# Optimization experiments

Measured on AMD Instinct MI355X. Metric: run time of the kernel, lower is better.

The kernel has to match this reference:

```python
import jax, jax.numpy as jnp
import numpy as np

HEADS = 4
DIM_HEAD = 32
DIM = 128
HIDDEN = HEADS * DIM_HEAD  # 128


def setup_inputs() -> dict:
    key = jax.random.key(0)
    k1, k2, k3, k4 = jax.random.split(key, 4)
    B, C, H, W = 8, DIM, 128, 128
    x = jax.random.normal(k1, (B, C, H, W), dtype=jnp.float32)
    # 1x1 conv weights stored as [out_ch, in_ch] (kernel dims squeezed)
    w_qkv = jax.random.normal(k2, (3 * HIDDEN, DIM), dtype=jnp.float32) * (1.0 / np.sqrt(DIM))
    w_out = jax.random.normal(k3, (DIM, HIDDEN), dtype=jnp.float32) * (1.0 / np.sqrt(HIDDEN))
    b_out = jax.random.normal(k4, (DIM,), dtype=jnp.float32) * 0.01
    return {"x": x, "w_qkv": w_qkv, "w_out": w_out, "b_out": b_out}


def reference(x, w_qkv, w_out, b_out):
    b, c, h, w = x.shape
    n = h * w
    # 1x1 conv == per-pixel matmul over channels
    qkv = jnp.einsum('bchw,oc->bohw', x, w_qkv)            # [b, 3*HIDDEN, h, w]
    # channel layout: (qkv, heads, dim_head)
    qkv = qkv.reshape(b, 3, HEADS, DIM_HEAD, n)            # [b, 3, H, d, n]
    q, k, v = qkv[:, 0], qkv[:, 1], qkv[:, 2]
    k = jax.nn.softmax(k, axis=-1)                         # softmax over spatial n
    context = jnp.einsum('bhdn,bhen->bhde', k, v)          # [b, H, d, d] (tiny)
    out = jnp.einsum('bhde,bhdn->bhen', context, q)        # [b, H, d, n]
    out = out.reshape(b, HIDDEN, h, w)
    y = jnp.einsum('bchw,oc->bohw', out, w_out) + b_out[None, :, None, None]
    return y
```

## Files before the change

kernel.cpp:

```cpp
#include <hip/hip_runtime.h>
#include <math.h>

#define C_ 128
#define N_ 16384

#define WS_Z    0
#define WS_CTX  1024
#define WS_BMAT 33792
#define WS_A    164864
#define WS_PCTX 295936
#define WS_PZ   (WS_PCTX + 1024*4096)
#define WS_END  (WS_PZ + 512*128)

typedef __attribute__((ext_vector_type(8))) short bf16x8;
typedef __attribute__((ext_vector_type(4))) float f32x4;
typedef __attribute__((ext_vector_type(4))) unsigned int u32x4;

__device__ __forceinline__ unsigned int pkbf(float a, float b) {
  unsigned int r;
  asm("v_cvt_pk_bf16_f32 %0, %1, %2" : "=v"(r) : "v"(a), "v"(b));
  return r;
}

__device__ __forceinline__ bf16x8 make_frag(float4 u, float4 v) {
  u32x4 q = {pkbf(u.x, u.y), pkbf(u.z, u.w), pkbf(v.x, v.y), pkbf(v.z, v.w)};
  return *(bf16x8*)&q;
}

__device__ __forceinline__ bf16x8 lds_frag(const unsigned short* p) {
  bf16x8 f;
  ((unsigned long long*)&f)[0] = ((const unsigned long long*)p)[0];
  ((unsigned long long*)&f)[1] = ((const unsigned long long*)p)[1];
  return f;
}

template<bool ATOMIC>
__global__ __launch_bounds__(512, 4) void k1_kv_ctx(const float* __restrict__ x,
                                                    const float* __restrict__ wqkv,
                                                    float* __restrict__ ws) {
  __shared__ __attribute__((aligned(16))) unsigned short smem[2 * 128 * 68];
#define XS(n, c)    smem[(n) * 132 + (c)]
#define EKV(t, r, c) smem[((t) * 128 + (r)) * 68 + (c)]
  const int tid  = threadIdx.x;
  const int wave = tid >> 6;
  const int l15  = tid & 15;
  const int l4   = (tid >> 4) & 3;
  const int b    = blockIdx.y;
  const int j    = blockIdx.x;
  const int h    = wave & 3;
  const int t    = wave >> 2;
  const int kvrow0 = h * 32 + t * 128;
  const float* xb = x + (size_t)b * ((size_t)C_ * N_);

  bf16x8 wf[2][4];
  #pragma unroll
  for (int mi = 0; mi < 2; ++mi)
    #pragma unroll
    for (int ki = 0; ki < 4; ++ki) {
      const float* p = wqkv + (size_t)(128 + kvrow0 + mi * 16 + l15) * C_ + ki * 32 + l4 * 8;
      wf[mi][ki] = make_frag(*(const float4*)p, *(const float4*)(p + 4));
    }

  const f32x4 z4 = {0.f, 0.f, 0.f, 0.f};
  f32x4 ctxacc[2][2];
  #pragma unroll
  for (int i = 0; i < 2; ++i)
    #pragma unroll
    for (int jj = 0; jj < 2; ++jj) ctxacc[i][jj] = z4;
  float zacc[2][4];
  #pragma unroll
  for (int i = 0; i < 2; ++i)
    #pragma unroll
    for (int r = 0; r < 4; ++r) zacc[i][r] = 0.f;

  for (int st = 0; st < 4; ++st) {
    const int nb = j * 256 + st * 64;
    __syncthreads();
    #pragma unroll
    for (int i = 0; i < 4; ++i) {
      int idx = tid + i * 512;
      int k = idx >> 4, n4 = idx & 15;
      float4 v = *(const float4*)(xb + (size_t)k * N_ + nb + n4 * 4);
      unsigned int p01 = pkbf(v.x, v.y), p23 = pkbf(v.z, v.w);
      XS(n4 * 4 + 0, k) = (unsigned short)p01;
      XS(n4 * 4 + 1, k) = (unsigned short)(p01 >> 16);
      XS(n4 * 4 + 2, k) = (unsigned short)p23;
      XS(n4 * 4 + 3, k) = (unsigned short)(p23 >> 16);
    }
    __syncthreads();

    f32x4 acc[2][4];
    #pragma unroll
    for (int mi = 0; mi < 2; ++mi)
      #pragma unroll
      for (int ni = 0; ni < 4; ++ni) acc[mi][ni] = z4;
    #pragma unroll
    for (int ki = 0; ki < 4; ++ki) {
      bf16x8 bfr[4];
      #pragma unroll
      for (int ni = 0; ni < 4; ++ni)
        bfr[ni] = lds_frag(&XS(ni * 16 + l15, ki * 32 + l4 * 8));
      #pragma unroll
      for (int mi = 0; mi < 2; ++mi)
        #pragma unroll
        for (int ni = 0; ni < 4; ++ni)
          acc[mi][ni] = __builtin_amdgcn_mfma_f32_16x16x32_bf16(
              wf[mi][ki], bfr[ni], acc[mi][ni], 0, 0, 0);
    }
    __syncthreads();

    #pragma unroll
    for (int mi = 0; mi < 2; ++mi) {
      int rb = h * 32 + mi * 16 + l4 * 4;
      #pragma unroll
      for (int ni = 0; ni < 4; ++ni) {
        int col = ni * 16 + l15;
        float e0, e1, e2, e3;
        if (t == 0) {
          e0 = __expf(acc[mi][ni][0]); e1 = __expf(acc[mi][ni][1]);
          e2 = __expf(acc[mi][ni][2]); e3 = __expf(acc[mi][ni][3]);
          zacc[mi][0] += e0; zacc[mi][1] += e1;
          zacc[mi][2] += e2; zacc[mi][3] += e3;
        } else {
          e0 = acc[mi][ni][0]; e1 = acc[mi][ni][1];
          e2 = acc[mi][ni][2]; e3 = acc[mi][ni][3];
        }
        unsigned int p01 = pkbf(e0, e1), p23 = pkbf(e2, e3);
        EKV(t, rb + 0, col) = (unsigned short)p01;
        EKV(t, rb + 1, col) = (unsigned short)(p01 >> 16);
        EKV(t, rb + 2, col) = (unsigned short)p23;
        EKV(t, rb + 3, col) = (unsigned short)(p23 >> 16);
      }
    }
    __syncthreads();

    {
      bf16x8 af[2], bfv[2];
      #pragma unroll
      for (int m2 = 0; m2 < 2; ++m2)
        af[m2] = lds_frag(&EKV(0, h * 32 + m2 * 16 + l15, t * 32 + l4 * 8));
      #pragma unroll
      for (int n2 = 0; n2 < 2; ++n2)
        bfv[n2] = lds_frag(&EKV(1, h * 32 + n2 * 16 + l15, t * 32 + l4 * 8));
      #pragma unroll
      for (int m2 = 0; m2 < 2; ++m2)
        #pragma unroll
        for (int n2 = 0; n2 < 2; ++n2)
          ctxacc[m2][n2] = __builtin_amdgcn_mfma_f32_16x16x32_bf16(
              af[m2], bfv[n2], ctxacc[m2][n2], 0, 0, 0);
    }
  }

  if (!ATOMIC) {
    float* ps = ws + WS_PCTX + (size_t)((b * 64 + j) * 2 + t) * 4096 + h * 1024;
    #pragma unroll
    for (int m2 = 0; m2 < 2; ++m2)
      #pragma unroll
      for (int n2 = 0; n2 < 2; ++n2)
        #pragma unroll
        for (int r = 0; r < 4; ++r)
          ps[(m2 * 16 + l4 * 4 + r) * 32 + n2 * 16 + l15] = ctxacc[m2][n2][r];
  } else {
    float* ctx = ws + WS_CTX + (size_t)(b * 4 + h) * 1024;
    #pragma unroll
    for (int m2 = 0; m2 < 2; ++m2)
      #pragma unroll
      for (int n2 = 0; n2 < 2; ++n2)
        #pragma unroll
        for (int r = 0; r < 4; ++r)
          atomicAdd(&ctx[(m2 * 16 + l4 * 4 + r) * 32 + n2 * 16 + l15],
                    ctxacc[m2][n2][r]);
  }
  if (t == 0) {
    #pragma unroll
    for (int mi = 0; mi < 2; ++mi)
      #pragma unroll
      for (int r = 0; r < 4; ++r) {
        float z = zacc[mi][r];
        z += __shfl_xor(z, 1);
        z += __shfl_xor(z, 2);
        z += __shfl_xor(z, 4);
        z += __shfl_xor(z, 8);
        if (l15 == 0) {
          int row = h * 32 + mi * 16 + l4 * 4 + r;
          if (!ATOMIC)
            ws[WS_PZ + (size_t)(b * 64 + j) * 128 + row] = z;
          else
            atomicAdd(&ws[WS_Z + b * 128 + row], z);
        }
      }
  }
#undef XS
#undef EKV
}

__global__ __launch_bounds__(256) void k1b(float* __restrict__ ws) {
  const int tid = threadIdx.x;
  const int eq = blockIdx.x;
  const int h  = blockIdx.y;
  const int b  = blockIdx.z;
  const int el = eq * 256 + tid;
  const float* p = ws + WS_PCTX + (size_t)(b * 128) * 4096 + h * 1024 + el;
  float s = 0.f;
  #pragma unroll 8
  for (int jj = 0; jj < 128; ++jj) s += p[(size_t)jj * 4096];
  ws[WS_CTX + (size_t)(b * 4 + h) * 1024 + el] = s;
  if (eq == 0 && tid < 32) {
    const float* pz = ws + WS_PZ + (size_t)(b * 64) * 128 + h * 32 + tid;
    float z = 0.f;
    #pragma unroll 8
    for (int jj = 0; jj < 64; ++jj) z += pz[(size_t)jj * 128];
    ws[WS_Z + b * 128 + h * 32 + tid] = z;
  }
}

__global__ __launch_bounds__(256) void k2a(const float* __restrict__ w_qkv,
                                           float* __restrict__ ws) {
  __shared__ float cn[32][33];
  __shared__ float wqs[32][128];
  const int tid = threadIdx.x;
  const int h = blockIdx.x, b = blockIdx.y;
  const float* Z   = ws + WS_Z + b * 128 + h * 32;
  const float* ctx = ws + WS_CTX + ((b * 4 + h) * 32) * 32;

  for (int k = 0; k < 4; ++k) {
    int idx = tid + k * 256;
    int d = idx >> 5, e = idx & 31;
    cn[d][e] = ctx[d * 32 + e] / Z[d];
  }
  for (int k = 0; k < 4; ++k) {
    int idx = tid + k * 256;
    int d = idx >> 5, f4 = idx & 31;
    *(float4*)&wqs[d][f4 * 4] = *(const float4*)(w_qkv + (h * 32 + d) * 128 + f4 * 4);
  }
  __syncthreads();

  const int e = tid >> 3, cs = (tid & 7) * 16;
  float s[16];
  #pragma unroll
  for (int jj = 0; jj < 16; ++jj) s[jj] = 0.f;
  for (int d = 0; d < 32; ++d) {
    float v = cn[d][e];
    #pragma unroll
    for (int jj = 0; jj < 16; ++jj) s[jj] = fmaf(v, wqs[d][cs + jj], s[jj]);
  }
  float* Bm = ws + WS_BMAT + ((size_t)b * 128 + h * 32 + e) * 128;
  #pragma unroll
  for (int jj = 0; jj < 16; ++jj) Bm[cs + jj] = s[jj];
}

__global__ __launch_bounds__(256) void k2b(const float* __restrict__ w_out,
                                           float* __restrict__ ws) {
  __shared__ float bs[128][128];
  __shared__ float wos[32][128];
  const int tid = threadIdx.x;
  const int oq = blockIdx.x, b = blockIdx.y;
  const float* Bm = ws + WS_BMAT + (size_t)b * 128 * 128;

  for (int k = 0; k < 16; ++k) {
    int idx = tid + k * 256;
    int r = idx >> 5, f4 = idx & 31;
    *(float4*)&bs[r][f4 * 4] = *(const float4*)(Bm + r * 128 + f4 * 4);
  }
  for (int k = 0; k < 4; ++k) {
    int idx = tid + k * 256;
    int r = idx >> 5, f4 = idx & 31;
    *(float4*)&wos[r][f4 * 4] = *(const float4*)(w_out + (oq * 32 + r) * 128 + f4 * 4);
  }
  __syncthreads();

  const int ol = tid >> 3, cq = (tid & 7) * 16;
  float s[16];
  #pragma unroll
  for (int jj = 0; jj < 16; ++jj) s[jj] = 0.f;
  for (int eg = 0; eg < 128; ++eg) {
    float w = wos[ol][eg];
    #pragma unroll
    for (int jj = 0; jj < 16; ++jj) s[jj] = fmaf(w, bs[eg][cq + jj], s[jj]);
  }
  float* A = ws + WS_A + ((size_t)b * 128 + oq * 32 + ol) * 128;
  #pragma unroll
  for (int jj = 0; jj < 16; ++jj) A[cq + jj] = s[jj];
}

__global__ __launch_bounds__(256, 4) void k3(const float* __restrict__ x,
                                             const float* __restrict__ bout,
                                             const float* __restrict__ ws,
                                             float* __restrict__ y) {
  __shared__ __attribute__((aligned(16))) unsigned short xs2[2][64][132];
  const int tid  = threadIdx.x;
  const int wave = tid >> 6;
  const int l15  = tid & 15;
  const int l4   = (tid >> 4) & 3;
  const int b    = blockIdx.y;
  const int n0   = blockIdx.x * 128;
  const float* xb = x + (size_t)b * ((size_t)C_ * N_);
  const float* A  = ws + WS_A + (size_t)b * 128 * 128;

  bf16x8 af[2][4];
  #pragma unroll
  for (int mi = 0; mi < 2; ++mi)
    #pragma unroll
    for (int ki = 0; ki < 4; ++ki) {
      const float* p = A + (size_t)(wave * 32 + mi * 16 + l15) * 128 + ki * 32 + l4 * 8;
      af[mi][ki] = make_frag(*(const float4*)p, *(const float4*)(p + 4));
    }
  float bias[2][4];
  #pragma unroll
  for (int mi = 0; mi < 2; ++mi)
    #pragma unroll
    for (int r = 0; r < 4; ++r)
      bias[mi][r] = bout[wave * 32 + mi * 16 + l4 * 4 + r];

  #pragma unroll
  for (int i = 0; i < 8; ++i) {
    int idx = tid + i * 256;
    int k = idx >> 4, n4 = idx & 15;
    float4 v = *(const float4*)(xb + (size_t)k * N_ + n0 + n4 * 4);
    unsigned int p01 = pkbf(v.x, v.y), p23 = pkbf(v.z, v.w);
    xs2[0][n4 * 4 + 0][k] = (unsigned short)p01;
    xs2[0][n4 * 4 + 1][k] = (unsigned short)(p01 >> 16);
    xs2[0][n4 * 4 + 2][k] = (unsigned short)p23;
    xs2[0][n4 * 4 + 3][k] = (unsigned short)(p23 >> 16);
  }
  __syncthreads();

  const f32x4 z4 = {0.f, 0.f, 0.f, 0.f};
  float* yb = y + (size_t)b * ((size_t)128 * N_);

  #pragma unroll
  for (int st = 0; st < 2; ++st) {
    const int nb = n0 + st * 64;
    f32x4 acc[2][4];
    #pragma unroll
    for (int mi = 0; mi < 2; ++mi)
      #pragma unroll
      for (int ni = 0; ni < 4; ++ni) acc[mi][ni] = z4;
    #pragma unroll
    for (int ki = 0; ki < 4; ++ki) {
      bf16x8 bfr[4];
      #pragma unroll
      for (int ni = 0; ni < 4; ++ni)
        bfr[ni] = lds_frag(&xs2[st][ni * 16 + l15][ki * 32 + l4 * 8]);
      #pragma unroll
      for (int mi = 0; mi < 2; ++mi)
        #pragma unroll
        for (int ni = 0; ni < 4; ++ni)
          acc[mi][ni] = __builtin_amdgcn_mfma_f32_16x16x32_bf16(
              af[mi][ki], bfr[ni], acc[mi][ni], 0, 0, 0);
    }

    if (st == 0) {
      #pragma unroll
      for (int i = 0; i < 8; ++i) {
        int idx = tid + i * 256;
        int k = idx >> 4, n4 = idx & 15;
        float4 v = *(const float4*)(xb + (size_t)k * N_ + n0 + 64 + n4 * 4);
        unsigned int p01 = pkbf(v.x, v.y), p23 = pkbf(v.z, v.w);
        xs2[1][n4 * 4 + 0][k] = (unsigned short)p01;
        xs2[1][n4 * 4 + 1][k] = (unsigned short)(p01 >> 16);
        xs2[1][n4 * 4 + 2][k] = (unsigned short)p23;
        xs2[1][n4 * 4 + 3][k] = (unsigned short)(p23 >> 16);
      }
    }

    #pragma unroll
    for (int mi = 0; mi < 2; ++mi)
      #pragma unroll
      for (int ni = 0; ni < 4; ++ni)
        #pragma unroll
        for (int r = 0; r < 4; ++r)
          yb[(size_t)(wave * 32 + mi * 16 + l4 * 4 + r) * N_ + nb + ni * 16 + l15] =
              acc[mi][ni][r] + bias[mi][r];

    if (st == 0) __syncthreads();
  }
}

extern "C" void kernel_launch(void* const* d_in, const int* in_sizes, int n_in,
                              void* d_out, int out_size, void* d_ws, size_t ws_size,
                              hipStream_t stream) {
  const float* x     = (const float*)d_in[0];
  const float* w_qkv = (const float*)d_in[1];
  const float* w_out = (const float*)d_in[2];
  const float* b_out = (const float*)d_in[3];
  float* y  = (float*)d_out;
  float* ws = (float*)d_ws;

  const bool partial = ws_size >= (size_t)WS_END * sizeof(float);
  if (partial) {
    k1_kv_ctx<false><<<dim3(64, 8), 512, 0, stream>>>(x, w_qkv, ws);
    k1b<<<dim3(4, 4, 8), 256, 0, stream>>>(ws);
  } else {
    hipMemsetAsync(ws, 0, (1024 + 32768) * sizeof(float), stream);
    k1_kv_ctx<true><<<dim3(64, 8), 512, 0, stream>>>(x, w_qkv, ws);
  }
  k2a<<<dim3(4, 8), 256, 0, stream>>>(w_qkv, ws);
  k2b<<<dim3(4, 8), 256, 0, stream>>>(w_out, ws);
  k3<<<dim3(128, 8), 256, 0, stream>>>(x, b_out, ws, y);
}
```

Measured before the change: 89.29 us.

## Swap MFMA operand order, vectorize LDS/global stores, prefetch x tiles in KV kernel

The MFMA operands are swapped so each lane holds four consecutive spatial outputs. This lets the exp(k)/v tile be written to LDS as 8-byte vectors and the final y output be written as float4 rows instead of scalar strided stores. The x tile transpose into LDS now packs four channels per 8-byte store, and LDS row padding changes to 136/72. The KV kernel register-prefetches the next x tile during compute, removes one barrier per step, and lowers its occupancy hint from 4 to 2 blocks per CU, which adds register pressure.

```diff
diff --git a/kernel.cpp b/kernel.cpp
--- a/kernel.cpp
+++ b/kernel.cpp
@@ -15,6 +15,7 @@
 typedef __attribute__((ext_vector_type(8))) short bf16x8;
 typedef __attribute__((ext_vector_type(4))) float f32x4;
 typedef __attribute__((ext_vector_type(4))) unsigned int u32x4;
+typedef __attribute__((ext_vector_type(2))) unsigned int u32x2;
 
 __device__ __forceinline__ unsigned int pkbf(float a, float b) {
   unsigned int r;
@@ -27,20 +28,22 @@
   return *(bf16x8*)&q;
 }
 
-__device__ __forceinline__ bf16x8 lds_frag(const unsigned short* p) {
-  bf16x8 f;
-  ((unsigned long long*)&f)[0] = ((const unsigned long long*)p)[0];
-  ((unsigned long long*)&f)[1] = ((const unsigned long long*)p)[1];
-  return f;
+__device__ __forceinline__ bf16x8 lds_frag16(const unsigned short* p) {
+  u32x4 q = *(const u32x4*)p;
+  return *(bf16x8*)&q;
+}
+
+__device__ __forceinline__ void load4(const float* p, float* o) {
+  float4 v = *(const float4*)p;
+  o[0] = v.x; o[1] = v.y; o[2] = v.z; o[3] = v.w;
 }
 
 template<bool ATOMIC>
-__global__ __launch_bounds__(512, 4) void k1_kv_ctx(const float* __restrict__ x,
+__global__ __launch_bounds__(512, 2) void k1_kv_ctx(const float* __restrict__ x,
                                                     const float* __restrict__ wqkv,
                                                     float* __restrict__ ws) {
-  __shared__ __attribute__((aligned(16))) unsigned short smem[2 * 128 * 68];
-#define XS(n, c)    smem[(n) * 132 + (c)]
-#define EKV(t, r, c) smem[((t) * 128 + (r)) * 68 + (c)]
+  __shared__ __attribute__((aligned(16))) unsigned short xs[64][136];
+  __shared__ __attribute__((aligned(16))) unsigned short ekv[2][128][72];
   const int tid  = threadIdx.x;
   const int wave = tid >> 6;
   const int l15  = tid & 15;
@@ -52,6 +55,9 @@
   const int kvrow0 = h * 32 + t * 128;
   const float* xb = x + (size_t)b * ((size_t)C_ * N_);
 
+  const int sn4 = tid & 15;
+  const int scq = tid >> 4;
+
   bf16x8 wf[2][4];
   #pragma unroll
   for (int mi = 0; mi < 2; ++mi)
@@ -61,94 +67,99 @@
       wf[mi][ki] = make_frag(*(const float4*)p, *(const float4*)(p + 4));
     }
 
+  {
+    float va[4][4];
+    #pragma unroll
+    for (int r = 0; r < 4; ++r)
+      load4(xb + (size_t)(scq * 4 + r) * N_ + j * 256 + sn4 * 4, va[r]);
+    #pragma unroll
+    for (int i = 0; i < 4; ++i) {
+      u32x2 w = {pkbf(va[0][i], va[1][i]), pkbf(va[2][i], va[3][i])};
+      *(u32x2*)&xs[sn4 * 4 + i][scq * 4] = w;
+    }
+  }
+  __syncthreads();
+
   const f32x4 z4 = {0.f, 0.f, 0.f, 0.f};
   f32x4 ctxacc[2][2];
   #pragma unroll
   for (int i = 0; i < 2; ++i)
     #pragma unroll
     for (int jj = 0; jj < 2; ++jj) ctxacc[i][jj] = z4;
-  float zacc[2][4];
-  #pragma unroll
-  for (int i = 0; i < 2; ++i)
-    #pragma unroll
-    for (int r = 0; r < 4; ++r) zacc[i][r] = 0.f;
+  float zacc[2] = {0.f, 0.f};
 
   for (int st = 0; st < 4; ++st) {
-    const int nb = j * 256 + st * 64;
+    float pf[4][4];
+    if (st < 3) {
+      const int nbn = j * 256 + (st + 1) * 64;
+      #pragma unroll
+      for (int r = 0; r < 4; ++r)
+        load4(xb + (size_t)(scq * 4 + r) * N_ + nbn + sn4 * 4, pf[r]);
+    }
+
+    #pragma unroll
+    for (int half = 0; half < 2; ++half) {
+      f32x4 acc[2][2];
+      #pragma unroll
+      for (int a = 0; a < 2; ++a)
+        #pragma unroll
+        for (int m = 0; m < 2; ++m) acc[a][m] = z4;
+      #pragma unroll
+      for (int ki = 0; ki < 4; ++ki) {
+        bf16x8 bfr[2];
+        #pragma unroll
+        for (int ni2 = 0; ni2 < 2; ++ni2)
+          bfr[ni2] = lds_frag16(&xs[half * 32 + ni2 * 16 + l15][ki * 32 + l4 * 8]);
+        #pragma unroll
+        for (int ni2 = 0; ni2 < 2; ++ni2)
+          #pragma unroll
+          for (int mi = 0; mi < 2; ++mi)
+            acc[ni2][mi] = __builtin_amdgcn_mfma_f32_16x16x32_bf16(
+                bfr[ni2], wf[mi][ki], acc[ni2][mi], 0, 0, 0);
+      }
+      #pragma unroll
+      for (int ni2 = 0; ni2 < 2; ++ni2)
+        #pragma unroll
+        for (int mi = 0; mi < 2; ++mi) {
+          float e0, e1, e2, e3;
+          if (t == 0) {
+            e0 = __expf(acc[ni2][mi][0]); e1 = __expf(acc[ni2][mi][1]);
+            e2 = __expf(acc[ni2][mi][2]); e3 = __expf(acc[ni2][mi][3]);
+            zacc[mi] += (e0 + e1) + (e2 + e3);
+          } else {
+            e0 = acc[ni2][mi][0]; e1 = acc[ni2][mi][1];
+            e2 = acc[ni2][mi][2]; e3 = acc[ni2][mi][3];
+          }
+          u32x2 w = {pkbf(e0, e1), pkbf(e2, e3)};
+          *(u32x2*)&ekv[t][h * 32 + mi * 16 + l15][(half * 2 + ni2) * 16 + l4 * 4] = w;
+        }
+    }
     __syncthreads();
-    #pragma unroll
-    for (int i = 0; i < 4; ++i) {
-      int idx = tid + i * 512;
-      int k = idx >> 4, n4 = idx & 15;
-      float4 v = *(const float4*)(xb + (size_t)k * N_ + nb + n4 * 4);
-      unsigned int p01 = pkbf(v.x, v.y), p23 = pkbf(v.z, v.w);
-      XS(n4 * 4 + 0, k) = (unsigned short)p01;
-      XS(n4 * 4 + 1, k) = (unsigned short)(p01 >> 16);
-      XS(n4 * 4 + 2, k) = (unsigned short)p23;
-      XS(n4 * 4 + 3, k) = (unsigned short)(p23 >> 16);
-    }
-    __syncthreads();
-
-    f32x4 acc[2][4];
-    #pragma unroll
-    for (int mi = 0; mi < 2; ++mi)
-      #pragma unroll
-      for (int ni = 0; ni < 4; ++ni) acc[mi][ni] = z4;
-    #pragma unroll
-    for (int ki = 0; ki < 4; ++ki) {
-      bf16x8 bfr[4];
-      #pragma unroll
-      for (int ni = 0; ni < 4; ++ni)
-        bfr[ni] = lds_frag(&XS(ni * 16 + l15, ki * 32 + l4 * 8));
-      #pragma unroll
-      for (int mi = 0; mi < 2; ++mi)
-        #pragma unroll
-        for (int ni = 0; ni < 4; ++ni)
-          acc[mi][ni] = __builtin_amdgcn_mfma_f32_16x16x32_bf16(
-              wf[mi][ki], bfr[ni], acc[mi][ni], 0, 0, 0);
-    }
-    __syncthreads();
-
-    #pragma unroll
-    for (int mi = 0; mi < 2; ++mi) {
-      int rb = h * 32 + mi * 16 + l4 * 4;
-      #pragma unroll
-      for (int ni = 0; ni < 4; ++ni) {
-        int col = ni * 16 + l15;
-        float e0, e1, e2, e3;
-        if (t == 0) {
-          e0 = __expf(acc[mi][ni][0]); e1 = __expf(acc[mi][ni][1]);
-          e2 = __expf(acc[mi][ni][2]); e3 = __expf(acc[mi][ni][3]);
-          zacc[mi][0] += e0; zacc[mi][1] += e1;
-          zacc[mi][2] += e2; zacc[mi][3] += e3;
-        } else {
-          e0 = acc[mi][ni][0]; e1 = acc[mi][ni][1];
-          e2 = acc[mi][ni][2]; e3 = acc[mi][ni][3];
-        }
-        unsigned int p01 = pkbf(e0, e1), p23 = pkbf(e2, e3);
-        EKV(t, rb + 0, col) = (unsigned short)p01;
-        EKV(t, rb + 1, col) = (unsigned short)(p01 >> 16);
-        EKV(t, rb + 2, col) = (unsigned short)p23;
-        EKV(t, rb + 3, col) = (unsigned short)(p23 >> 16);
-      }
-    }
-    __syncthreads();
 
     {
-      bf16x8 af[2], bfv[2];
+      bf16x8 af2[2], bv2[2];
       #pragma unroll
       for (int m2 = 0; m2 < 2; ++m2)
-        af[m2] = lds_frag(&EKV(0, h * 32 + m2 * 16 + l15, t * 32 + l4 * 8));
+        af2[m2] = lds_frag16(&ekv[0][h * 32 + m2 * 16 + l15][t * 32 + l4 * 8]);
       #pragma unroll
       for (int n2 = 0; n2 < 2; ++n2)
-        bfv[n2] = lds_frag(&EKV(1, h * 32 + n2 * 16 + l15, t * 32 + l4 * 8));
+        bv2[n2] = lds_frag16(&ekv[1][h * 32 + n2 * 16 + l15][t * 32 + l4 * 8]);
       #pragma unroll
       for (int m2 = 0; m2 < 2; ++m2)
         #pragma unroll
         for (int n2 = 0; n2 < 2; ++n2)
           ctxacc[m2][n2] = __builtin_amdgcn_mfma_f32_16x16x32_bf16(
-              af[m2], bfv[n2], ctxacc[m2][n2], 0, 0, 0);
-    }
+              af2[m2], bv2[n2], ctxacc[m2][n2], 0, 0, 0);
+    }
+
+    if (st < 3) {
+      #pragma unroll
+      for (int i = 0; i < 4; ++i) {
+        u32x2 w = {pkbf(pf[0][i], pf[1][i]), pkbf(pf[2][i], pf[3][i])};
+        *(u32x2*)&xs[sn4 * 4 + i][scq * 4] = w;
+      }
+    }
+    __syncthreads();
   }
 
   if (!ATOMIC) {
@@ -173,25 +184,19 @@
   }
   if (t == 0) {
     #pragma unroll
-    for (int mi = 0; mi < 2; ++mi)
-      #pragma unroll
-      for (int r = 0; r < 4; ++r) {
-        float z = zacc[mi][r];
-        z += __shfl_xor(z, 1);
-        z += __shfl_xor(z, 2);
-        z += __shfl_xor(z, 4);
-        z += __shfl_xor(z, 8);
-        if (l15 == 0) {
-          int row = h * 32 + mi * 16 + l4 * 4 + r;
-          if (!ATOMIC)
-            ws[WS_PZ + (size_t)(b * 64 + j) * 128 + row] = z;
-          else
-            atomicAdd(&ws[WS_Z + b * 128 + row], z);
-        }
+    for (int mi = 0; mi < 2; ++mi) {
+      float z = zacc[mi];
+      z += __shfl_xor(z, 16);
+      z += __shfl_xor(z, 32);
+      if ((tid & 48) == 0) {
+        int row = h * 32 + mi * 16 + l15;
+        if (!ATOMIC)
+          ws[WS_PZ + (size_t)(b * 64 + j) * 128 + row] = z;
+        else
+          atomicAdd(&ws[WS_Z + b * 128 + row], z);
       }
-  }
-#undef XS
-#undef EKV
+    }
+  }
 }
 
 __global__ __launch_bounds__(256) void k1b(float* __restrict__ ws) {
@@ -287,7 +292,7 @@
                                              const float* __restrict__ bout,
                                              const float* __restrict__ ws,
                                              float* __restrict__ y) {
-  __shared__ __attribute__((aligned(16))) unsigned short xs2[2][64][132];
+  __shared__ __attribute__((aligned(16))) unsigned short xs2[2][64][136];
   const int tid  = threadIdx.x;
   const int wave = tid >> 6;
   const int l15  = tid & 15;
@@ -305,23 +310,23 @@
       const float* p = A + (size_t)(wave * 32 + mi * 16 + l15) * 128 + ki * 32 + l4 * 8;
       af[mi][ki] = make_frag(*(const float4*)p, *(const float4*)(p + 4));
     }
-  float bias[2][4];
-  #pragma unroll
-  for (int mi = 0; mi < 2; ++mi)
+  float bias[2];
+  #pragma unroll
+  for (int mi = 0; mi < 2; ++mi) bias[mi] = bout[wave * 32 + mi * 16 + l15];
+
+  #pragma unroll
+  for (int it = 0; it < 2; ++it) {
+    int idx = tid + it * 256;
+    int n4 = idx & 15, cq = idx >> 4;
+    float va[4][4];
     #pragma unroll
     for (int r = 0; r < 4; ++r)
-      bias[mi][r] = bout[wave * 32 + mi * 16 + l4 * 4 + r];
-
-  #pragma unroll
-  for (int i = 0; i < 8; ++i) {
-    int idx = tid + i * 256;
-    int k = idx >> 4, n4 = idx & 15;
-    float4 v = *(const float4*)(xb + (size_t)k * N_ + n0 + n4 * 4);
-    unsigned int p01 = pkbf(v.x, v.y), p23 = pkbf(v.z, v.w);
-    xs2[0][n4 * 4 + 0][k] = (unsigned short)p01;
-    xs2[0][n4 * 4 + 1][k] = (unsigned short)(p01 >> 16);
-    xs2[0][n4 * 4 + 2][k] = (unsigned short)p23;
-    xs2[0][n4 * 4 + 3][k] = (unsigned short)(p23 >> 16);
+      load4(xb + (size_t)(cq * 4 + r) * N_ + n0 + n4 * 4, va[r]);
+    #pragma unroll
+    for (int i = 0; i < 4; ++i) {
+      u32x2 w = {pkbf(va[0][i], va[1][i]), pkbf(va[2][i], va[3][i])};
+      *(u32x2*)&xs2[0][n4 * 4 + i][cq * 4] = w;
+    }
   }
   __syncthreads();
 
@@ -331,47 +336,53 @@
   #pragma unroll
   for (int st = 0; st < 2; ++st) {
     const int nb = n0 + st * 64;
-    f32x4 acc[2][4];
-    #pragma unroll
-    for (int mi = 0; mi < 2; ++mi)
-      #pragma unroll
-      for (int ni = 0; ni < 4; ++ni) acc[mi][ni] = z4;
+    f32x4 acc[4][2];
+    #pragma unroll
+    for (int ni = 0; ni < 4; ++ni)
+      #pragma unroll
+      for (int mi = 0; mi < 2; ++mi) acc[ni][mi] = z4;
     #pragma unroll
     for (int ki = 0; ki < 4; ++ki) {
       bf16x8 bfr[4];
       #pragma unroll
       for (int ni = 0; ni < 4; ++ni)
-        bfr[ni] = lds_frag(&xs2[st][ni * 16 + l15][ki * 32 + l4 * 8]);
-      #pragma unroll
-      for (int mi = 0; mi < 2; ++mi)
-        #pragma unroll
-        for (int ni = 0; ni < 4; ++ni)
-          acc[mi][ni] = __builtin_amdgcn_mfma_f32_16x16x32_bf16(
-              af[mi][ki], bfr[ni], acc[mi][ni], 0, 0, 0);
+        bfr[ni] = lds_frag16(&xs2[st][ni * 16 + l15][ki * 32 + l4 * 8]);
+      #pragma unroll
+      for (int ni = 0; ni < 4; ++ni)
+        #pragma unroll
+        for (int mi = 0; mi < 2; ++mi)
+          acc[ni][mi] = __builtin_amdgcn_mfma_f32_16x16x32_bf16(
+              bfr[ni], af[mi][ki], acc[ni][mi], 0, 0, 0);
     }
 
     if (st == 0) {
       #pragma unroll
-      for (int i = 0; i < 8; ++i) {
-        int idx = tid + i * 256;
-        int k = idx >> 4, n4 = idx & 15;
-        float4 v = *(const float4*)(xb + (size_t)k * N_ + n0 + 64 + n4 * 4);
-        unsigned int p01 = pkbf(v.x, v.y), p23 = pkbf(v.z, v.w);
-        xs2[1][n4 * 4 + 0][k] = (unsigned short)p01;
-        xs2[1][n4 * 4 + 1][k] = (unsigned short)(p01 >> 16);
-        xs2[1][n4 * 4 + 2][k] = (unsigned short)p23;
-        xs2[1][n4 * 4 + 3][k] = (unsigned short)(p23 >> 16);
+      for (int it = 0; it < 2; ++it) {
+        int idx = tid + it * 256;
+        int n4 = idx & 15, cq = idx >> 4;
+        float va[4][4];
+        #pragma unroll
+        for (int r = 0; r < 4; ++r)
+          load4(xb + (size_t)(cq * 4 + r) * N_ + n0 + 64 + n4 * 4, va[r]);
+        #pragma unroll
+        for (int i = 0; i < 4; ++i) {
+          u32x2 w = {pkbf(va[0][i], va[1][i]), pkbf(va[2][i], va[3][i])};
+          *(u32x2*)&xs2[1][n4 * 4 + i][cq * 4] = w;
+        }
       }
     }
 
     #pragma unroll
-    for (int mi = 0; mi < 2; ++mi)
-      #pragma unroll
-      for (int ni = 0; ni < 4; ++ni)
-        #pragma unroll
-        for (int r = 0; r < 4; ++r)
-          yb[(size_t)(wave * 32 + mi * 16 + l4 * 4 + r) * N_ + nb + ni * 16 + l15] =
-              acc[mi][ni][r] + bias[mi][r];
+    for (int ni = 0; ni < 4; ++ni)
+      #pragma unroll
+      for (int mi = 0; mi < 2; ++mi) {
+        float4 o;
+        o.x = acc[ni][mi][0] + bias[mi];
+        o.y = acc[ni][mi][1] + bias[mi];
+        o.z = acc[ni][mi][2] + bias[mi];
+        o.w = acc[ni][mi][3] + bias[mi];
+        *(float4*)(yb + (size_t)(wave * 32 + mi * 16 + l15) * N_ + nb + ni * 16 + l4 * 4) = o;
+      }
 
     if (st == 0) __syncthreads();
   }
```

After: 79.89 us. 10.5% less time.
